# Kernel optimization log

Measured on AMD Instinct MI355X. Metric: run time of the kernel, lower is better.

Reference implementation:

```python
import jax, jax.numpy as jnp
import numpy as np

TIME_STEP = 7


def _grid_sample_3d(vol, grid):
    """Trilinear 3D grid_sample, padding_mode='border', align_corners=True.
    vol:  [B, C, D, H, W]
    grid: [B, D, H, W, 3] with last dim (x, y, z) == (W, H, D) coords in [-1, 1].
    """
    B, C, D, H, W = vol.shape

    def unnorm(c, size):
        # align_corners=True mapping, then border clamp
        c = (c + 1.0) * 0.5 * (size - 1)
        return jnp.clip(c, 0.0, size - 1.0)

    x = unnorm(grid[..., 0], W)  # [B,D,H,W]
    y = unnorm(grid[..., 1], H)
    z = unnorm(grid[..., 2], D)

    x0f = jnp.floor(x); y0f = jnp.floor(y); z0f = jnp.floor(z)
    wx = (x - x0f)[:, None]  # [B,1,D,H,W] for broadcast over channels
    wy = (y - y0f)[:, None]
    wz = (z - z0f)[:, None]

    x0 = x0f.astype(jnp.int32); x1 = jnp.minimum(x0 + 1, W - 1)
    y0 = y0f.astype(jnp.int32); y1 = jnp.minimum(y0 + 1, H - 1)
    z0 = z0f.astype(jnp.int32); z1 = jnp.minimum(z0 + 1, D - 1)

    def gather(zi, yi, xi):
        # per-batch fancy gather -> [B, C, D, H, W]
        return jax.vmap(lambda v, zz, yy, xx: v[:, zz, yy, xx])(vol, zi, yi, xi)

    c000 = gather(z0, y0, x0); c001 = gather(z0, y0, x1)
    c010 = gather(z0, y1, x0); c011 = gather(z0, y1, x1)
    c100 = gather(z1, y0, x0); c101 = gather(z1, y0, x1)
    c110 = gather(z1, y1, x0); c111 = gather(z1, y1, x1)

    out = ((c000 * (1 - wx) + c001 * wx) * (1 - wy) + (c010 * (1 - wx) + c011 * wx) * wy) * (1 - wz) \
        + ((c100 * (1 - wx) + c101 * wx) * (1 - wy) + (c110 * (1 - wx) + c111 * wx) * wy) * wz
    return out


def setup_inputs() -> dict:
    key = jax.random.key(0)
    flow = jax.random.normal(key, (1, 3, 192, 192, 192), dtype=jnp.float32)
    return {"flow": flow}


def reference(flow) -> jnp.ndarray:
    B, C, D, H, W = flow.shape
    gd, gh, gw = jnp.meshgrid(
        jnp.linspace(-1.0, 1.0, D, dtype=jnp.float32),
        jnp.linspace(-1.0, 1.0, H, dtype=jnp.float32),
        jnp.linspace(-1.0, 1.0, W, dtype=jnp.float32),
        indexing="ij",
    )
    flow = flow / (2.0 ** TIME_STEP)
    for _ in range(TIME_STEP):
        disp_d = gd + flow[:, 0]  # [B,D,H,W]
        disp_h = gh + flow[:, 1]
        disp_w = gw + flow[:, 2]
        deformation = jnp.stack((disp_w, disp_h, disp_d), axis=-1)  # (x,y,z)
        flow = flow + _grid_sample_3d(flow, deformation)
    return flow
```

## Files before the change

kernel.cpp:

```cpp
#include <hip/hip_runtime.h>


constexpr int DD = 192, HH = 192, WW = 192;
constexpr int NN = DD * HH * WW;
constexpr int NB = NN / 256;
constexpr int NXCD = 8;
constexpr int CHUNK = NB / NXCD;
constexpr int TT = WW / 2;

struct F3 { float x, y, z; };
typedef float f4 __attribute__((ext_vector_type(4)));

__device__ __forceinline__ int rec_addr(int z, int y, int x) {
    return ((((z >> 1) * TT + (y >> 1)) * TT + (x >> 1)) << 3)
         + (((z & 1) << 2) | ((y & 1) << 1) | (x & 1));
}

template <int SM, int DM>
__global__ __launch_bounds__(256) void diffeo_step(
    const void* __restrict__ srcv, void* __restrict__ dstv, float scale)
{
    int bid = blockIdx.x;
    int swz = (bid & (NXCD - 1)) * CHUNK + (bid >> 3);
    int gid = swz * 256 + threadIdx.x;

    int w, h, d;
    if constexpr (SM == 1 || DM == 1) {
        int slot = gid & 7;
        int tile = gid >> 3;
        int tx = tile % TT;
        int t2 = tile / TT;
        int ty = t2 % TT;
        int tz = t2 / TT;
        w = (tx << 1) | (slot & 1);
        h = (ty << 1) | ((slot >> 1) & 1);
        d = (tz << 1) | (slot >> 2);
    } else {
        w = gid % WW;
        int t = gid / WW;
        h = t % HH;
        d = t / HH;
    }
    int idx = (d * HH + h) * WW + w;

    float f0, f1, f2;
    if constexpr (SM == 0) {
        const float* src = (const float*)srcv;
        f0 = src[idx] * scale;
        f1 = src[idx + NN] * scale;
        f2 = src[idx + 2 * NN] * scale;
    } else if constexpr (SM == 1) {
        const f4* s4 = (const f4*)srcv;
        f4 own = s4[gid];
        f0 = own.x * scale; f1 = own.y * scale; f2 = own.z * scale;
    } else {
        const F3* s3 = (const F3*)srcv;
        F3 own = s3[gid];
        f0 = own.x * scale; f1 = own.y * scale; f2 = own.z * scale;
    }

    float x = fminf(fmaxf((float)w + f2 * (0.5f * (WW - 1)), 0.0f), (float)(WW - 1));
    float y = fminf(fmaxf((float)h + f1 * (0.5f * (HH - 1)), 0.0f), (float)(HH - 1));
    float z = fminf(fmaxf((float)d + f0 * (0.5f * (DD - 1)), 0.0f), (float)(DD - 1));

    int x0 = (int)x;  float wx = x - (float)x0;
    int y0 = (int)y;  float wy = y - (float)y0;
    int z0 = (int)z;  float wz = z - (float)z0;
    int x1 = min(x0 + 1, WW - 1);
    int y1 = min(y0 + 1, HH - 1);
    int z1 = min(z0 + 1, DD - 1);

    float ox = 1.0f - wx, oy = 1.0f - wy, oz = 1.0f - wz;
    float w000 = ox * oy * oz, w001 = wx * oy * oz;
    float w010 = ox * wy * oz, w011 = wx * wy * oz;
    float w100 = ox * oy * wz, w101 = wx * oy * wz;
    float w110 = ox * wy * wz, w111 = wx * wy * wz;

    float v0, v1, v2;
    if constexpr (SM == 0) {
        const float* src = (const float*)srcv;
        int i000 = (z0 * HH + y0) * WW + x0, i001 = (z0 * HH + y0) * WW + x1;
        int i010 = (z0 * HH + y1) * WW + x0, i011 = (z0 * HH + y1) * WW + x1;
        int i100 = (z1 * HH + y0) * WW + x0, i101 = (z1 * HH + y0) * WW + x1;
        int i110 = (z1 * HH + y1) * WW + x0, i111 = (z1 * HH + y1) * WW + x1;
        float acc[3];
#pragma unroll
        for (int c = 0; c < 3; ++c) {
            const float* s = src + c * NN;
            acc[c] =
                w000 * s[i000] + w001 * s[i001] +
                w010 * s[i010] + w011 * s[i011] +
                w100 * s[i100] + w101 * s[i101] +
                w110 * s[i110] + w111 * s[i111];
        }
        v0 = acc[0]; v1 = acc[1]; v2 = acc[2];
    } else if constexpr (SM == 1) {
        const f4* s4 = (const f4*)srcv;
        int a000 = rec_addr(z0, y0, x0), a001 = rec_addr(z0, y0, x1);
        int a010 = rec_addr(z0, y1, x0), a011 = rec_addr(z0, y1, x1);
        int a100 = rec_addr(z1, y0, x0), a101 = rec_addr(z1, y0, x1);
        int a110 = rec_addr(z1, y1, x0), a111 = rec_addr(z1, y1, x1);
        f4 c000 = s4[a000];
        f4 c001 = s4[a001];
        f4 c010 = s4[a010];
        f4 c011 = s4[a011];
        f4 c100 = s4[a100];
        f4 c101 = s4[a101];
        f4 c110 = s4[a110];
        f4 c111 = s4[a111];
        asm volatile("" : "+v"(c000), "+v"(c001), "+v"(c010), "+v"(c011),
                          "+v"(c100), "+v"(c101), "+v"(c110), "+v"(c111));
        v0 = w000 * c000.x + w001 * c001.x + w010 * c010.x + w011 * c011.x
           + w100 * c100.x + w101 * c101.x + w110 * c110.x + w111 * c111.x;
        v1 = w000 * c000.y + w001 * c001.y + w010 * c010.y + w011 * c011.y
           + w100 * c100.y + w101 * c101.y + w110 * c110.y + w111 * c111.y;
        v2 = w000 * c000.z + w001 * c001.z + w010 * c010.z + w011 * c011.z
           + w100 * c100.z + w101 * c101.z + w110 * c110.z + w111 * c111.z;
    } else {
        const F3* s3 = (const F3*)srcv;
        int i000 = (z0 * HH + y0) * WW + x0, i001 = (z0 * HH + y0) * WW + x1;
        int i010 = (z0 * HH + y1) * WW + x0, i011 = (z0 * HH + y1) * WW + x1;
        int i100 = (z1 * HH + y0) * WW + x0, i101 = (z1 * HH + y0) * WW + x1;
        int i110 = (z1 * HH + y1) * WW + x0, i111 = (z1 * HH + y1) * WW + x1;
        F3 c000 = s3[i000], c001 = s3[i001], c010 = s3[i010], c011 = s3[i011];
        F3 c100 = s3[i100], c101 = s3[i101], c110 = s3[i110], c111 = s3[i111];
        v0 = w000 * c000.x + w001 * c001.x + w010 * c010.x + w011 * c011.x
           + w100 * c100.x + w101 * c101.x + w110 * c110.x + w111 * c111.x;
        v1 = w000 * c000.y + w001 * c001.y + w010 * c010.y + w011 * c011.y
           + w100 * c100.y + w101 * c101.y + w110 * c110.y + w111 * c111.y;
        v2 = w000 * c000.z + w001 * c001.z + w010 * c010.z + w011 * c011.z
           + w100 * c100.z + w101 * c101.z + w110 * c110.z + w111 * c111.z;
    }

    float o0 = f0 + scale * v0;
    float o1 = f1 + scale * v1;
    float o2 = f2 + scale * v2;
    if constexpr (DM == 0) {
        float* dst = (float*)dstv;
        dst[idx] = o0; dst[idx + NN] = o1; dst[idx + 2 * NN] = o2;
    } else if constexpr (DM == 1) {
        f4* d4 = (f4*)dstv;
        f4 o = { o0, o1, o2, 0.0f };
        d4[gid] = o;
    } else {
        F3* d3 = (F3*)dstv;
        F3 o = { o0, o1, o2 };
        d3[gid] = o;
    }
}

extern "C" void kernel_launch(void* const* d_in, const int* in_sizes, int n_in,
                              void* d_out, int out_size, void* d_ws, size_t ws_size,
                              hipStream_t stream) {
    const void* in = d_in[0];
    void* out = d_out;
    const float inv = 1.0f / 128.0f;

    if (ws_size >= (size_t)NN * 32) {
        f4* qa = (f4*)d_ws;
        f4* qb = (f4*)d_ws + NN;
        diffeo_step<0, 1><<<NB, 256, 0, stream>>>(in, qa, inv);
        diffeo_step<1, 1><<<NB, 256, 0, stream>>>(qa, qb, 1.0f);
        diffeo_step<1, 1><<<NB, 256, 0, stream>>>(qb, qa, 1.0f);
        diffeo_step<1, 1><<<NB, 256, 0, stream>>>(qa, qb, 1.0f);
        diffeo_step<1, 1><<<NB, 256, 0, stream>>>(qb, qa, 1.0f);
        diffeo_step<1, 1><<<NB, 256, 0, stream>>>(qa, qb, 1.0f);
        diffeo_step<1, 0><<<NB, 256, 0, stream>>>(qb, out, 1.0f);
    } else {
        void* ws = d_ws;
        diffeo_step<0, 2><<<NB, 256, 0, stream>>>(in,  out, inv);
        diffeo_step<2, 2><<<NB, 256, 0, stream>>>(out, ws,  1.0f);
        diffeo_step<2, 2><<<NB, 256, 0, stream>>>(ws,  out, 1.0f);
        diffeo_step<2, 2><<<NB, 256, 0, stream>>>(out, ws,  1.0f);
        diffeo_step<2, 2><<<NB, 256, 0, stream>>>(ws,  out, 1.0f);
        diffeo_step<2, 2><<<NB, 256, 0, stream>>>(out, ws,  1.0f);
        diffeo_step<2, 0><<<NB, 256, 0, stream>>>(ws,  out, 1.0f);
    }
}
```

Measured before the change: 650.3 us.

## Use x-duplicated paired-row layout so trilinear gathers need four corner pairs

Introduces a new intermediate layout in which each voxel is stored next to its +x neighbour, with rows interleaved in y-pairs. Each sample now reads four adjacent 32-byte f4 pairs instead of eight scattered f4 loads, and the x lerp runs on f4 vectors. Writes are duplicated into the neighbour slot, which doubles workspace and store traffic. Blocks of 384 threads map to two y-rows of one z-slice with XCD swizzling, and the old float3 fallback path is removed.

Result: no change. 649.8 us (-0.1%).

```diff
diff --git a/kernel.cpp b/kernel.cpp
--- a/kernel.cpp
+++ b/kernel.cpp
@@ -3,13 +3,134 @@
 
 constexpr int DD = 192, HH = 192, WW = 192;
 constexpr int NN = DD * HH * WW;
+constexpr int NXCD = 8;
+constexpr int HP = HH / 2;
+constexpr int NBX = DD * HP;
+constexpr int CHUNKX = NBX / NXCD;
 constexpr int NB = NN / 256;
-constexpr int NXCD = 8;
 constexpr int CHUNK = NB / NXCD;
 constexpr int TT = WW / 2;
 
-struct F3 { float x, y, z; };
 typedef float f4 __attribute__((ext_vector_type(4)));
+constexpr float INV = 1.0f / 128.0f;
+
+__device__ __forceinline__ int xdup_L(int z, int y, int x) {
+    return ((z * HP + (y >> 1)) * WW + x) * 2 + (y & 1);
+}
+
+struct Pos {
+    int x0, y0, z0, x1, y1, z1;
+    float wx, wy, wz;
+};
+
+__device__ __forceinline__ Pos posn(int w, int h, int d, float f0, float f1, float f2) {
+    Pos p;
+    float x = fminf(fmaxf((float)w + f2 * (0.5f * (WW - 1)), 0.0f), (float)(WW - 1));
+    float y = fminf(fmaxf((float)h + f1 * (0.5f * (HH - 1)), 0.0f), (float)(HH - 1));
+    float z = fminf(fmaxf((float)d + f0 * (0.5f * (DD - 1)), 0.0f), (float)(DD - 1));
+    p.x0 = (int)x; p.wx = x - (float)p.x0;
+    p.y0 = (int)y; p.wy = y - (float)p.y0;
+    p.z0 = (int)z; p.wz = z - (float)p.z0;
+    p.x1 = min(p.x0 + 1, WW - 1);
+    p.y1 = min(p.y0 + 1, HH - 1);
+    p.z1 = min(p.z0 + 1, DD - 1);
+    return p;
+}
+
+__device__ __forceinline__ f4 xdup_sample(const f4* __restrict__ src, const Pos& p) {
+    int L00 = xdup_L(p.z0, p.y0, p.x0);
+    int L01 = xdup_L(p.z0, p.y1, p.x0);
+    int L10 = xdup_L(p.z1, p.y0, p.x0);
+    int L11 = xdup_L(p.z1, p.y1, p.x0);
+    f4 a0 = src[2 * L00], a1 = src[2 * L00 + 1];
+    f4 b0 = src[2 * L01], b1 = src[2 * L01 + 1];
+    f4 c0 = src[2 * L10], c1 = src[2 * L10 + 1];
+    f4 d0 = src[2 * L11], d1 = src[2 * L11 + 1];
+    asm volatile("" : "+v"(a0), "+v"(a1), "+v"(b0), "+v"(b1),
+                      "+v"(c0), "+v"(c1), "+v"(d0), "+v"(d1));
+    float ox = 1.0f - p.wx, oy = 1.0f - p.wy, oz = 1.0f - p.wz;
+    f4 r00 = a0 * ox + a1 * p.wx;
+    f4 r01 = b0 * ox + b1 * p.wx;
+    f4 r10 = c0 * ox + c1 * p.wx;
+    f4 r11 = d0 * ox + d1 * p.wx;
+    return (r00 * oy + r01 * p.wy) * oz + (r10 * oy + r11 * p.wy) * p.wz;
+}
+
+__device__ __forceinline__ void xdup_store(f4* __restrict__ dst, int L, int x, f4 o) {
+    dst[2 * L] = o;
+    if (x > 0)       dst[2 * L - 3] = o;
+    if (x == WW - 1) dst[2 * L + 1] = o;
+}
+
+__device__ __forceinline__ void xdup_decode(int bid, int tid,
+                                            int& z, int& y, int& x, int& L) {
+    int swz = (bid & (NXCD - 1)) * CHUNKX + (bid >> 3);
+    z = swz / HP;
+    int yp = swz - z * HP;
+    int p = tid & 1;
+    x = tid >> 1;
+    y = 2 * yp + p;
+    L = (swz * WW + x) * 2 + p;
+}
+
+__global__ __launch_bounds__(384) void diffeo_in_x(
+    const float* __restrict__ src, f4* __restrict__ dst)
+{
+    int z, y, x, L;
+    xdup_decode(blockIdx.x, threadIdx.x, z, y, x, L);
+    int idx = (z * HH + y) * WW + x;
+
+    float f0 = src[idx] * INV;
+    float f1 = src[idx + NN] * INV;
+    float f2 = src[idx + 2 * NN] * INV;
+    Pos p = posn(x, y, z, f0, f1, f2);
+
+    int i000 = (p.z0 * HH + p.y0) * WW + p.x0, i001 = (p.z0 * HH + p.y0) * WW + p.x1;
+    int i010 = (p.z0 * HH + p.y1) * WW + p.x0, i011 = (p.z0 * HH + p.y1) * WW + p.x1;
+    int i100 = (p.z1 * HH + p.y0) * WW + p.x0, i101 = (p.z1 * HH + p.y0) * WW + p.x1;
+    int i110 = (p.z1 * HH + p.y1) * WW + p.x0, i111 = (p.z1 * HH + p.y1) * WW + p.x1;
+    float ox = 1.0f - p.wx, oy = 1.0f - p.wy, oz = 1.0f - p.wz;
+    float w000 = ox * oy * oz, w001 = p.wx * oy * oz;
+    float w010 = ox * p.wy * oz, w011 = p.wx * p.wy * oz;
+    float w100 = ox * oy * p.wz, w101 = p.wx * oy * p.wz;
+    float w110 = ox * p.wy * p.wz, w111 = p.wx * p.wy * p.wz;
+    float v[3];
+#pragma unroll
+    for (int c = 0; c < 3; ++c) {
+        const float* s = src + c * NN;
+        v[c] = w000 * s[i000] + w001 * s[i001] + w010 * s[i010] + w011 * s[i011]
+             + w100 * s[i100] + w101 * s[i101] + w110 * s[i110] + w111 * s[i111];
+    }
+    f4 o = { f0 + INV * v[0], f1 + INV * v[1], f2 + INV * v[2], 0.0f };
+    xdup_store(dst, L, x, o);
+}
+
+__global__ __launch_bounds__(384) void diffeo_mid_x(
+    const f4* __restrict__ src, f4* __restrict__ dst)
+{
+    int z, y, x, L;
+    xdup_decode(blockIdx.x, threadIdx.x, z, y, x, L);
+    f4 own = src[2 * L];
+    Pos p = posn(x, y, z, own.x, own.y, own.z);
+    f4 vv = xdup_sample(src, p);
+    f4 o = own + vv;
+    o.w = 0.0f;
+    xdup_store(dst, L, x, o);
+}
+
+__global__ __launch_bounds__(384) void diffeo_out_x(
+    const f4* __restrict__ src, float* __restrict__ dst)
+{
+    int z, y, x, L;
+    xdup_decode(blockIdx.x, threadIdx.x, z, y, x, L);
+    int idx = (z * HH + y) * WW + x;
+    f4 own = src[2 * L];
+    Pos p = posn(x, y, z, own.x, own.y, own.z);
+    f4 vv = xdup_sample(src, p);
+    dst[idx]          = own.x + vv.x;
+    dst[idx + NN]     = own.y + vv.y;
+    dst[idx + 2 * NN] = own.z + vv.z;
+}
 
 __device__ __forceinline__ int rec_addr(int z, int y, int x) {
     return ((((z >> 1) * TT + (y >> 1)) * TT + (x >> 1)) << 3)
@@ -25,7 +146,7 @@
     int gid = swz * 256 + threadIdx.x;
 
     int w, h, d;
-    if constexpr (SM == 1 || DM == 1) {
+    {
         int slot = gid & 7;
         int tile = gid >> 3;
         int tx = tile % TT;
@@ -35,79 +156,45 @@
         w = (tx << 1) | (slot & 1);
         h = (ty << 1) | ((slot >> 1) & 1);
         d = (tz << 1) | (slot >> 2);
-    } else {
-        w = gid % WW;
-        int t = gid / WW;
-        h = t % HH;
-        d = t / HH;
     }
     int idx = (d * HH + h) * WW + w;
 
-    float f0, f1, f2;
+    f4 own;
     if constexpr (SM == 0) {
         const float* src = (const float*)srcv;
-        f0 = src[idx] * scale;
-        f1 = src[idx + NN] * scale;
-        f2 = src[idx + 2 * NN] * scale;
-    } else if constexpr (SM == 1) {
-        const f4* s4 = (const f4*)srcv;
-        f4 own = s4[gid];
-        f0 = own.x * scale; f1 = own.y * scale; f2 = own.z * scale;
-    } else {
-        const F3* s3 = (const F3*)srcv;
-        F3 own = s3[gid];
-        f0 = own.x * scale; f1 = own.y * scale; f2 = own.z * scale;
-    }
-
-    float x = fminf(fmaxf((float)w + f2 * (0.5f * (WW - 1)), 0.0f), (float)(WW - 1));
-    float y = fminf(fmaxf((float)h + f1 * (0.5f * (HH - 1)), 0.0f), (float)(HH - 1));
-    float z = fminf(fmaxf((float)d + f0 * (0.5f * (DD - 1)), 0.0f), (float)(DD - 1));
-
-    int x0 = (int)x;  float wx = x - (float)x0;
-    int y0 = (int)y;  float wy = y - (float)y0;
-    int z0 = (int)z;  float wz = z - (float)z0;
-    int x1 = min(x0 + 1, WW - 1);
-    int y1 = min(y0 + 1, HH - 1);
-    int z1 = min(z0 + 1, DD - 1);
-
-    float ox = 1.0f - wx, oy = 1.0f - wy, oz = 1.0f - wz;
-    float w000 = ox * oy * oz, w001 = wx * oy * oz;
-    float w010 = ox * wy * oz, w011 = wx * wy * oz;
-    float w100 = ox * oy * wz, w101 = wx * oy * wz;
-    float w110 = ox * wy * wz, w111 = wx * wy * wz;
+        own = f4{ src[idx], src[idx + NN], src[idx + 2 * NN], 0.0f };
+    } else {
+        own = ((const f4*)srcv)[gid];
+    }
+    float f0 = own.x * scale, f1 = own.y * scale, f2 = own.z * scale;
+    Pos p = posn(w, h, d, f0, f1, f2);
+    float ox = 1.0f - p.wx, oy = 1.0f - p.wy, oz = 1.0f - p.wz;
+    float w000 = ox * oy * oz, w001 = p.wx * oy * oz;
+    float w010 = ox * p.wy * oz, w011 = p.wx * p.wy * oz;
+    float w100 = ox * oy * p.wz, w101 = p.wx * oy * p.wz;
+    float w110 = ox * p.wy * p.wz, w111 = p.wx * p.wy * p.wz;
 
     float v0, v1, v2;
     if constexpr (SM == 0) {
         const float* src = (const float*)srcv;
-        int i000 = (z0 * HH + y0) * WW + x0, i001 = (z0 * HH + y0) * WW + x1;
-        int i010 = (z0 * HH + y1) * WW + x0, i011 = (z0 * HH + y1) * WW + x1;
-        int i100 = (z1 * HH + y0) * WW + x0, i101 = (z1 * HH + y0) * WW + x1;
-        int i110 = (z1 * HH + y1) * WW + x0, i111 = (z1 * HH + y1) * WW + x1;
+        int i000 = (p.z0 * HH + p.y0) * WW + p.x0, i001 = (p.z0 * HH + p.y0) * WW + p.x1;
+        int i010 = (p.z0 * HH + p.y1) * WW + p.x0, i011 = (p.z0 * HH + p.y1) * WW + p.x1;
+        int i100 = (p.z1 * HH + p.y0) * WW + p.x0, i101 = (p.z1 * HH + p.y0) * WW + p.x1;
+        int i110 = (p.z1 * HH + p.y1) * WW + p.x0, i111 = (p.z1 * HH + p.y1) * WW + p.x1;
         float acc[3];
 #pragma unroll
         for (int c = 0; c < 3; ++c) {
             const float* s = src + c * NN;
-            acc[c] =
-                w000 * s[i000] + w001 * s[i001] +
-                w010 * s[i010] + w011 * s[i011] +
-                w100 * s[i100] + w101 * s[i101] +
-                w110 * s[i110] + w111 * s[i111];
+            acc[c] = w000 * s[i000] + w001 * s[i001] + w010 * s[i010] + w011 * s[i011]
+                   + w100 * s[i100] + w101 * s[i101] + w110 * s[i110] + w111 * s[i111];
         }
         v0 = acc[0]; v1 = acc[1]; v2 = acc[2];
-    } else if constexpr (SM == 1) {
+    } else {
         const f4* s4 = (const f4*)srcv;
-        int a000 = rec_addr(z0, y0, x0), a001 = rec_addr(z0, y0, x1);
-        int a010 = rec_addr(z0, y1, x0), a011 = rec_addr(z0, y1, x1);
-        int a100 = rec_addr(z1, y0, x0), a101 = rec_addr(z1, y0, x1);
-        int a110 = rec_addr(z1, y1, x0), a111 = rec_addr(z1, y1, x1);
-        f4 c000 = s4[a000];
-        f4 c001 = s4[a001];
-        f4 c010 = s4[a010];
-        f4 c011 = s4[a011];
-        f4 c100 = s4[a100];
-        f4 c101 = s4[a101];
-        f4 c110 = s4[a110];
-        f4 c111 = s4[a111];
+        f4 c000 = s4[rec_addr(p.z0, p.y0, p.x0)], c001 = s4[rec_addr(p.z0, p.y0, p.x1)];
+        f4 c010 = s4[rec_addr(p.z0, p.y1, p.x0)], c011 = s4[rec_addr(p.z0, p.y1, p.x1)];
+        f4 c100 = s4[rec_addr(p.z1, p.y0, p.x0)], c101 = s4[rec_addr(p.z1, p.y0, p.x1)];
+        f4 c110 = s4[rec_addr(p.z1, p.y1, p.x0)], c111 = s4[rec_addr(p.z1, p.y1, p.x1)];
         asm volatile("" : "+v"(c000), "+v"(c001), "+v"(c010), "+v"(c011),
                           "+v"(c100), "+v"(c101), "+v"(c110), "+v"(c111));
         v0 = w000 * c000.x + w001 * c001.x + w010 * c010.x + w011 * c011.x
@@ -116,36 +203,14 @@
            + w100 * c100.y + w101 * c101.y + w110 * c110.y + w111 * c111.y;
         v2 = w000 * c000.z + w001 * c001.z + w010 * c010.z + w011 * c011.z
            + w100 * c100.z + w101 * c101.z + w110 * c110.z + w111 * c111.z;
-    } else {
-        const F3* s3 = (const F3*)srcv;
-        int i000 = (z0 * HH + y0) * WW + x0, i001 = (z0 * HH + y0) * WW + x1;
-        int i010 = (z0 * HH + y1) * WW + x0, i011 = (z0 * HH + y1) * WW + x1;
-        int i100 = (z1 * HH + y0) * WW + x0, i101 = (z1 * HH + y0) * WW + x1;
-        int i110 = (z1 * HH + y1) * WW + x0, i111 = (z1 * HH + y1) * WW + x1;
-        F3 c000 = s3[i000], c001 = s3[i001], c010 = s3[i010], c011 = s3[i011];
-        F3 c100 = s3[i100], c101 = s3[i101], c110 = s3[i110], c111 = s3[i111];
-        v0 = w000 * c000.x + w001 * c001.x + w010 * c010.x + w011 * c011.x
-           + w100 * c100.x + w101 * c101.x + w110 * c110.x + w111 * c111.x;
-        v1 = w000 * c000.y + w001 * c001.y + w010 * c010.y + w011 * c011.y
-           + w100 * c100.y + w101 * c101.y + w110 * c110.y + w111 * c111.y;
-        v2 = w000 * c000.z + w001 * c001.z + w010 * c010.z + w011 * c011.z
-           + w100 * c100.z + w101 * c101.z + w110 * c110.z + w111 * c111.z;
-    }
-
-    float o0 = f0 + scale * v0;
-    float o1 = f1 + scale * v1;
-    float o2 = f2 + scale * v2;
+    }
+
+    f4 o = { f0 + scale * v0, f1 + scale * v1, f2 + scale * v2, 0.0f };
     if constexpr (DM == 0) {
         float* dst = (float*)dstv;
-        dst[idx] = o0; dst[idx + NN] = o1; dst[idx + 2 * NN] = o2;
-    } else if constexpr (DM == 1) {
-        f4* d4 = (f4*)dstv;
-        f4 o = { o0, o1, o2, 0.0f };
-        d4[gid] = o;
-    } else {
-        F3* d3 = (F3*)dstv;
-        F3 o = { o0, o1, o2 };
-        d3[gid] = o;
+        dst[idx] = o.x; dst[idx + NN] = o.y; dst[idx + 2 * NN] = o.z;
+    } else {
+        ((f4*)dstv)[gid] = o;
     }
 }
 
@@ -154,26 +219,26 @@
                               hipStream_t stream) {
     const void* in = d_in[0];
     void* out = d_out;
-    const float inv = 1.0f / 128.0f;
-
-    if (ws_size >= (size_t)NN * 32) {
+
+    if (ws_size >= (size_t)NN * 64) {
+        f4* qa = (f4*)d_ws;
+        f4* qb = (f4*)d_ws + 2 * NN;
+        diffeo_in_x <<<NBX, 384, 0, stream>>>((const float*)in, qa);
+        diffeo_mid_x<<<NBX, 384, 0, stream>>>(qa, qb);
+        diffeo_mid_x<<<NBX, 384, 0, stream>>>(qb, qa);
+        diffeo_mid_x<<<NBX, 384, 0, stream>>>(qa, qb);
+        diffeo_mid_x<<<NBX, 384, 0, stream>>>(qb, qa);
+        diffeo_mid_x<<<NBX, 384, 0, stream>>>(qa, qb);
+        diffeo_out_x<<<NBX, 384, 0, stream>>>(qb, (float*)out);
+    } else {
         f4* qa = (f4*)d_ws;
         f4* qb = (f4*)d_ws + NN;
-        diffeo_step<0, 1><<<NB, 256, 0, stream>>>(in, qa, inv);
+        diffeo_step<0, 1><<<NB, 256, 0, stream>>>(in, qa, INV);
         diffeo_step<1, 1><<<NB, 256, 0, stream>>>(qa, qb, 1.0f);
         diffeo_step<1, 1><<<NB, 256, 0, stream>>>(qb, qa, 1.0f);
         diffeo_step<1, 1><<<NB, 256, 0, stream>>>(qa, qb, 1.0f);
         diffeo_step<1, 1><<<NB, 256, 0, stream>>>(qb, qa, 1.0f);
         diffeo_step<1, 1><<<NB, 256, 0, stream>>>(qa, qb, 1.0f);
         diffeo_step<1, 0><<<NB, 256, 0, stream>>>(qb, out, 1.0f);
-    } else {
-        void* ws = d_ws;
-        diffeo_step<0, 2><<<NB, 256, 0, stream>>>(in,  out, inv);
-        diffeo_step<2, 2><<<NB, 256, 0, stream>>>(out, ws,  1.0f);
-        diffeo_step<2, 2><<<NB, 256, 0, stream>>>(ws,  out, 1.0f);
-        diffeo_step<2, 2><<<NB, 256, 0, stream>>>(out, ws,  1.0f);
-        diffeo_step<2, 2><<<NB, 256, 0, stream>>>(ws,  out, 1.0f);
-        diffeo_step<2, 2><<<NB, 256, 0, stream>>>(out, ws,  1.0f);
-        diffeo_step<2, 0><<<NB, 256, 0, stream>>>(ws,  out, 1.0f);
-    }
-}
+    }
+}
```
